# Kernel tuning notes

Measured on AMD Instinct MI355X. Metric: run time of the kernel, lower is better.

Reference implementation:

```python
import jax, jax.numpy as jnp
import numpy as np
from jax import lax

NUM_STEPS = 20
BATCH, DIM, HID = 4096, 512, 2048


def setup_inputs() -> dict:
    key = jax.random.key(0)
    k_z, k_w1, k_w2 = jax.random.split(key, 3)
    z0 = jax.random.normal(k_z, (BATCH, DIM), dtype=jnp.float32)
    # fan-in scaled weights so the ODE dynamics stay well-conditioned
    W1 = jax.random.normal(k_w1, (DIM + 1, HID), dtype=jnp.float32) * (1.0 / np.sqrt(DIM + 1))
    b1 = jnp.zeros((HID,), dtype=jnp.float32)
    W2 = jax.random.normal(k_w2, (HID, DIM), dtype=jnp.float32) * (0.1 / np.sqrt(HID))
    b2 = jnp.zeros((DIM,), dtype=jnp.float32)
    t0 = jnp.zeros((), dtype=jnp.float32)
    t1 = jnp.ones((), dtype=jnp.float32)
    return {"z0": z0, "W1": W1, "b1": b1, "W2": W2, "b2": b2, "t0": t0, "t1": t1}


def reference(z0, W1, b1, W2, b2, t0, t1):
    h = (t1 - t0) / NUM_STEPS

    def func(z, t):
        # time broadcast to [batch, 1], concatenated to the state (Neural-ODE MLP dynamics)
        tb = jnp.full((z.shape[0], 1), t, dtype=z.dtype)
        hidden = jnp.tanh(jnp.concatenate([z, tb], axis=-1) @ W1 + b1)
        return hidden @ W2 + b2

    def step(z, i):
        t = t0 + i * h
        k1 = func(z, t)
        k2 = func(z + 0.5 * h * k1, t + 0.5 * h)
        k3 = func(z + 0.5 * h * k2, t + 0.5 * h)
        k4 = func(z + h * k3, t + h)
        z_next = z + (h / 6.0) * (k1 + 2.0 * k2 + 2.0 * k3 + k4)
        return z_next, None

    z, _ = lax.scan(step, z0, jnp.arange(NUM_STEPS, dtype=z0.dtype))
    return z
```

## Files before the change

kernel.cpp:

```cpp
#include <hip/hip_runtime.h>
#include <hip/hip_bf16.h>

#define BATCH 4096
#define DIM   512
#define HID   2048
#define NSTEPS 20

typedef __attribute__((ext_vector_type(8))) short short8;
typedef __attribute__((ext_vector_type(4))) short short4v;
typedef __attribute__((ext_vector_type(4))) float floatx4;

#define GLL(dst, src) __builtin_amdgcn_global_load_lds( \
    (const __attribute__((address_space(1))) void*)(src), \
    (__attribute__((address_space(3))) void*)(dst), 16, 0, 0)

__device__ __forceinline__ short f2bf(float x) {
    union { float f; unsigned u; } v; v.f = x;
    unsigned r = v.u + 0x7fffu + ((v.u >> 16) & 1u);
    return (short)(r >> 16);
}

__device__ __forceinline__ float fast_tanh(float x) {
    float e = __builtin_amdgcn_exp2f(x * 2.8853900817779268f);
    float r = __builtin_amdgcn_rcpf(1.0f + e);
    return 1.0f - 2.0f * r;
}

__global__ void transpose_cvt(const float* __restrict__ src, short* __restrict__ dst,
                              int K, int N) {
    __shared__ float tile[32][33];
    int k0 = blockIdx.x * 32, n0 = blockIdx.y * 32;
    int tx = threadIdx.x, ty = threadIdx.y;
    #pragma unroll
    for (int r = ty; r < 32; r += 8)
        tile[r][tx] = src[(size_t)(k0 + r) * N + n0 + tx];
    __syncthreads();
    #pragma unroll
    for (int r = ty; r < 32; r += 8)
        dst[(size_t)(n0 + r) * K + k0 + tx] = f2bf(tile[tx][r]);
}

__global__ void extract_row(const float* __restrict__ W1, float* __restrict__ w1last) {
    int i = blockIdx.x * 256 + threadIdx.x;
    w1last[i] = W1[(size_t)DIM * HID + i];
}

__global__ void init_abuf(const float* __restrict__ z0, short* __restrict__ abuf) {
    size_t i = (size_t)(blockIdx.x * 256 + threadIdx.x) * 4;
    float4 zv = *(const float4*)(z0 + i);
    short4v o;
    o[0] = f2bf(zv.x); o[1] = f2bf(zv.y); o[2] = f2bf(zv.z); o[3] = f2bf(zv.w);
    *(short4v*)(abuf + i) = o;
}

__global__ __launch_bounds__(256, 2)
void gemm1_tanh(const short* __restrict__ A, const short* __restrict__ Bt,
                const float* __restrict__ b1, const float* __restrict__ w1last,
                const float* __restrict__ t0p, const float* __restrict__ t1p,
                float c_t, float step_i,
                short* __restrict__ hidden) {
    __shared__ short Alds[128 * 128];
    __shared__ short Blds[128 * 128];
    const int tid = threadIdx.x;
    const int lane = tid & 63;
    const int wave = tid >> 6;
    const int wm = wave >> 1, wn = wave & 1;
    const int bm0 = blockIdx.x * 128;
    const int bn0 = blockIdx.y * 128;

    const float t0 = t0p[0], t1 = t1p[0];
    const float h = (t1 - t0) / (float)NSTEPS;
    const float teval = t0 + (step_i + c_t) * h;

    floatx4 acc[4][4];
    #pragma unroll
    for (int i = 0; i < 4; i++)
        #pragma unroll
        for (int j = 0; j < 4; j++) acc[i][j] = (floatx4)0.f;

    const int fr = lane & 15;
    const int fkc = lane >> 4;
    const int rx = fr & 7;

    for (int kk = 0; kk < DIM; kk += 128) {
        #pragma unroll
        for (int p = 0; p < 8; p++) {
            int c = tid + p * 256;
            int row = c >> 4;
            int ci = c & 15;
            int g = ((ci & 7) ^ (row & 7)) | (ci & 8);
            GLL(&Alds[c * 8], A  + (size_t)(bm0 + row) * DIM + kk + g * 8);
            GLL(&Blds[c * 8], Bt + (size_t)(bn0 + row) * DIM + kk + g * 8);
        }
        __syncthreads();
        #pragma unroll
        for (int s = 0; s < 4; s++) {
            const int lc = s * 4 + fkc;
            const int slot = ((((lc & 7) ^ rx) | (lc & 8))) * 8;
            short8 af[4], bfr[4];
            #pragma unroll
            for (int mt = 0; mt < 4; mt++)
                af[mt] = *(const short8*)&Alds[(wm * 64 + mt * 16 + fr) * 128 + slot];
            #pragma unroll
            for (int nt = 0; nt < 4; nt++)
                bfr[nt] = *(const short8*)&Blds[(wn * 64 + nt * 16 + fr) * 128 + slot];
            #pragma unroll
            for (int mt = 0; mt < 4; mt++)
                #pragma unroll
                for (int nt = 0; nt < 4; nt++)
                    acc[mt][nt] = __builtin_amdgcn_mfma_f32_16x16x32_bf16(bfr[nt], af[mt], acc[mt][nt], 0, 0, 0);
        }
        __syncthreads();
    }
    #pragma unroll
    for (int mt = 0; mt < 4; mt++) {
        int m = bm0 + wm * 64 + mt * 16 + fr;
        short* hrow = hidden + (size_t)m * HID;
        #pragma unroll
        for (int nt = 0; nt < 4; nt++) {
            int n0 = bn0 + wn * 64 + nt * 16 + fkc * 4;
            float4 bb = *(const float4*)&b1[n0];
            float4 wl = *(const float4*)&w1last[n0];
            short4v o;
            o[0] = f2bf(fast_tanh(acc[mt][nt][0] + bb.x + teval * wl.x));
            o[1] = f2bf(fast_tanh(acc[mt][nt][1] + bb.y + teval * wl.y));
            o[2] = f2bf(fast_tanh(acc[mt][nt][2] + bb.z + teval * wl.z));
            o[3] = f2bf(fast_tanh(acc[mt][nt][3] + bb.w + teval * wl.w));
            *(short4v*)&hrow[n0] = o;
        }
    }
}

__global__ __launch_bounds__(512, 2)
void gemm2_fused(const short* __restrict__ hidden,
                 const short* __restrict__ Bt,
                 const float* __restrict__ b2,
                 float* __restrict__ z,
                 float* __restrict__ kacc, short* __restrict__ abuf,
                 const float* __restrict__ t0p, const float* __restrict__ t1p,
                 int mode, float wk, float alpha_c) {
    __shared__ short lds[8 * 8192];
    const int tid = threadIdx.x;
    const int lane = tid & 63;
    const int wave = tid >> 6;
    const int bm0 = blockIdx.x * 64;
    const int bn0 = blockIdx.y * 64;
    const int kbase = wave * 256;

    short* slabA = &lds[wave * 8192];
    short* slabB = slabA + 4096;

    const int fr = lane & 15;
    const int fkc = lane >> 4;
    const int rx = fr & 7;
    const int l3 = lane >> 3;
    const int gch = (lane & 7) ^ l3;

    floatx4 acc[4][4];
    #pragma unroll
    for (int i = 0; i < 4; i++)
        #pragma unroll
        for (int j = 0; j < 4; j++) acc[i][j] = (floatx4)0.f;

    #pragma unroll
    for (int it = 0; it < 4; ++it) {
        const int k0 = kbase + it * 64;
        __builtin_amdgcn_s_waitcnt(0xC07F);
        #pragma unroll
        for (int j = 0; j < 8; j++) {
            int row = j * 8 + l3;
            GLL(&slabA[j * 512 + lane * 8], hidden + (size_t)(bm0 + row) * HID + k0 + gch * 8);
            GLL(&slabB[j * 512 + lane * 8], Bt     + (size_t)(bn0 + row) * HID + k0 + gch * 8);
        }
        __builtin_amdgcn_sched_barrier(0);
        __builtin_amdgcn_s_waitcnt(0x0F70);
        __builtin_amdgcn_sched_barrier(0);
        #pragma unroll
        for (int s = 0; s < 2; s++) {
            const int slot = ((s * 4 + fkc) ^ rx) * 8;
            short8 af[4], bfr[4];
            #pragma unroll
            for (int mt = 0; mt < 4; mt++)
                af[mt] = *(const short8*)&slabA[(mt * 16 + fr) * 64 + slot];
            #pragma unroll
            for (int nt = 0; nt < 4; nt++)
                bfr[nt] = *(const short8*)&slabB[(nt * 16 + fr) * 64 + slot];
            #pragma unroll
            for (int mt = 0; mt < 4; mt++)
                #pragma unroll
                for (int nt = 0; nt < 4; nt++)
                    acc[mt][nt] = __builtin_amdgcn_mfma_f32_16x16x32_bf16(af[mt], bfr[nt], acc[mt][nt], 0, 0, 0);
        }
        __builtin_amdgcn_sched_barrier(0);
    }

    float* fslab = (float*)slabA;
    #pragma unroll
    for (int mt = 0; mt < 4; mt++)
        #pragma unroll
        for (int nt = 0; nt < 4; nt++)
            #pragma unroll
            for (int r = 0; r < 4; r++) {
                int row = mt * 16 + fkc * 4 + r;
                int col = nt * 16 + fr;
                fslab[row * 64 + col] = acc[mt][nt][r];
            }
    __syncthreads();

    const int rrow = tid >> 3;
    const int c8 = (tid & 7) * 8;
    float4 v0 = make_float4(0.f, 0.f, 0.f, 0.f);
    float4 v1 = make_float4(0.f, 0.f, 0.f, 0.f);
    #pragma unroll
    for (int w = 0; w < 8; w++) {
        const float* fs = (const float*)&lds[w * 8192];
        float4 p0 = *(const float4*)&fs[rrow * 64 + c8];
        float4 p1 = *(const float4*)&fs[rrow * 64 + c8 + 4];
        v0.x += p0.x; v0.y += p0.y; v0.z += p0.z; v0.w += p0.w;
        v1.x += p1.x; v1.y += p1.y; v1.z += p1.z; v1.w += p1.w;
    }

    const float h = (t1p[0] - t0p[0]) / (float)NSTEPS;
    const float ah = alpha_c * h;
    const float h6 = h / 6.0f;
    const size_t base = (size_t)(bm0 + rrow) * DIM + bn0 + c8;
    float4 bb0 = *(const float4*)&b2[bn0 + c8];
    float4 bb1 = *(const float4*)&b2[bn0 + c8 + 4];
    float kv[8] = { v0.x + bb0.x, v0.y + bb0.y, v0.z + bb0.z, v0.w + bb0.w,
                    v1.x + bb1.x, v1.y + bb1.y, v1.z + bb1.z, v1.w + bb1.w };
    float4 zv0 = *(const float4*)&z[base];
    float4 zv1 = *(const float4*)&z[base + 4];
    float zl[8] = { zv0.x, zv0.y, zv0.z, zv0.w, zv1.x, zv1.y, zv1.z, zv1.w };
    float zn[8];
    if (mode == 0) {
        *(float4*)&kacc[base]     = make_float4(kv[0], kv[1], kv[2], kv[3]);
        *(float4*)&kacc[base + 4] = make_float4(kv[4], kv[5], kv[6], kv[7]);
        #pragma unroll
        for (int i = 0; i < 8; i++) zn[i] = zl[i] + ah * kv[i];
    } else if (mode == 1) {
        float4 ka0 = *(const float4*)&kacc[base];
        float4 ka1 = *(const float4*)&kacc[base + 4];
        *(float4*)&kacc[base]     = make_float4(ka0.x + wk * kv[0], ka0.y + wk * kv[1],
                                                ka0.z + wk * kv[2], ka0.w + wk * kv[3]);
        *(float4*)&kacc[base + 4] = make_float4(ka1.x + wk * kv[4], ka1.y + wk * kv[5],
                                                ka1.z + wk * kv[6], ka1.w + wk * kv[7]);
        #pragma unroll
        for (int i = 0; i < 8; i++) zn[i] = zl[i] + ah * kv[i];
    } else {
        float4 ka0 = *(const float4*)&kacc[base];
        float4 ka1 = *(const float4*)&kacc[base + 4];
        float kaf[8] = { ka0.x, ka0.y, ka0.z, ka0.w, ka1.x, ka1.y, ka1.z, ka1.w };
        #pragma unroll
        for (int i = 0; i < 8; i++) zn[i] = zl[i] + h6 * (kaf[i] + kv[i]);
        *(float4*)&z[base]     = make_float4(zn[0], zn[1], zn[2], zn[3]);
        *(float4*)&z[base + 4] = make_float4(zn[4], zn[5], zn[6], zn[7]);
    }
    short4v o0, o1;
    o0[0] = f2bf(zn[0]); o0[1] = f2bf(zn[1]); o0[2] = f2bf(zn[2]); o0[3] = f2bf(zn[3]);
    o1[0] = f2bf(zn[4]); o1[1] = f2bf(zn[5]); o1[2] = f2bf(zn[6]); o1[3] = f2bf(zn[7]);
    *(short4v*)&abuf[base]     = o0;
    *(short4v*)&abuf[base + 4] = o1;
}

extern "C" void kernel_launch(void* const* d_in, const int* in_sizes, int n_in,
                              void* d_out, int out_size, void* d_ws, size_t ws_size,
                              hipStream_t stream) {
    const float* z0  = (const float*)d_in[0];
    const float* W1  = (const float*)d_in[1];
    const float* b1  = (const float*)d_in[2];
    const float* W2  = (const float*)d_in[3];
    const float* b2  = (const float*)d_in[4];
    const float* t0p = (const float*)d_in[5];
    const float* t1p = (const float*)d_in[6];
    float* z = (float*)d_out;

    char* ws = (char*)d_ws;
    short* W1t    = (short*)(ws);
    short* W2t    = (short*)(ws + (2u << 20));
    float* w1last = (float*)(ws + (4u << 20));
    short* abuf   = (short*)(ws + (4u << 20) + (1u << 16));
    short* hidden = (short*)(ws + (8u << 20) + (1u << 16));
    float* kacc   = (float*)(ws + (24u << 20) + (1u << 16));

    hipMemcpyAsync(z, z0, (size_t)BATCH * DIM * sizeof(float),
                   hipMemcpyDeviceToDevice, stream);
    transpose_cvt<<<dim3(DIM / 32, HID / 32), dim3(32, 8), 0, stream>>>(W1, W1t, DIM, HID);
    transpose_cvt<<<dim3(HID / 32, DIM / 32), dim3(32, 8), 0, stream>>>(W2, W2t, HID, DIM);
    extract_row<<<HID / 256, 256, 0, stream>>>(W1, w1last);
    init_abuf<<<BATCH * DIM / 4 / 256, 256, 0, stream>>>(z0, abuf);

    const dim3 g1(BATCH / 128, HID / 128), g2(BATCH / 64, DIM / 64);
    const dim3 b1d(256), b2d(512);
    for (int i = 0; i < NSTEPS; i++) {
        float fi = (float)i;
        gemm1_tanh<<<g1, b1d, 0, stream>>>(abuf, W1t, b1, w1last, t0p, t1p, 0.0f, fi, hidden);
        gemm2_fused<<<g2, b2d, 0, stream>>>(hidden, W2t, b2, z, kacc, abuf, t0p, t1p, 0, 1.0f, 0.5f);
        gemm1_tanh<<<g1, b1d, 0, stream>>>(abuf, W1t, b1, w1last, t0p, t1p, 0.5f, fi, hidden);
        gemm2_fused<<<g2, b2d, 0, stream>>>(hidden, W2t, b2, z, kacc, abuf, t0p, t1p, 1, 2.0f, 0.5f);
        gemm1_tanh<<<g1, b1d, 0, stream>>>(abuf, W1t, b1, w1last, t0p, t1p, 0.5f, fi, hidden);
        gemm2_fused<<<g2, b2d, 0, stream>>>(hidden, W2t, b2, z, kacc, abuf, t0p, t1p, 1, 2.0f, 1.0f);
        gemm1_tanh<<<g1, b1d, 0, stream>>>(abuf, W1t, b1, w1last, t0p, t1p, 1.0f, fi, hidden);
        gemm2_fused<<<g2, b2d, 0, stream>>>(hidden, W2t, b2, z, kacc, abuf, t0p, t1p, 2, 1.0f, 0.0f);
    }
}
```

Before: 2.958 ms.

## Halve gemm2 LDS footprint to fit more blocks per CU

The split-K gemm2 kernel now stages K-chunks of 32 instead of 64 per wave, which halves its LDS allocation. It also splits the cross-wave reduction epilogue into two column halves that reuse the smaller slabs, and raises the launch-bounds occupancy hint from 2 to 4 blocks. The aim is to fit more resident blocks per CU and hide global-load latency. In exchange there are twice as many load/wait iterations, an extra barrier, and the XOR swizzle is dropped, which may cause LDS bank conflicts on the fragment reads.

After: 3.394 ms. 1.15x slower.

```diff
diff --git a/kernel.cpp b/kernel.cpp
--- a/kernel.cpp
+++ b/kernel.cpp
@@ -131,7 +131,7 @@
     }
 }
 
-__global__ __launch_bounds__(512, 2)
+__global__ __launch_bounds__(512, 4)
 void gemm2_fused(const short* __restrict__ hidden,
                  const short* __restrict__ Bt,
                  const float* __restrict__ b2,
@@ -139,7 +139,7 @@
                  float* __restrict__ kacc, short* __restrict__ abuf,
                  const float* __restrict__ t0p, const float* __restrict__ t1p,
                  int mode, float wk, float alpha_c) {
-    __shared__ short lds[8 * 8192];
+    __shared__ short lds[8 * 4096];
     const int tid = threadIdx.x;
     const int lane = tid & 63;
     const int wave = tid >> 6;
@@ -147,14 +147,11 @@
     const int bn0 = blockIdx.y * 64;
     const int kbase = wave * 256;
 
-    short* slabA = &lds[wave * 8192];
-    short* slabB = slabA + 4096;
+    short* slabA = &lds[wave * 4096];
+    short* slabB = slabA + 2048;
 
     const int fr = lane & 15;
     const int fkc = lane >> 4;
-    const int rx = fr & 7;
-    const int l3 = lane >> 3;
-    const int gch = (lane & 7) ^ l3;
 
     floatx4 acc[4][4];
     #pragma unroll
@@ -163,28 +160,28 @@
         for (int j = 0; j < 4; j++) acc[i][j] = (floatx4)0.f;
 
     #pragma unroll
-    for (int it = 0; it < 4; ++it) {
-        const int k0 = kbase + it * 64;
+    for (int it = 0; it < 8; ++it) {
+        const int k0 = kbase + it * 32;
         __builtin_amdgcn_s_waitcnt(0xC07F);
         #pragma unroll
-        for (int j = 0; j < 8; j++) {
-            int row = j * 8 + l3;
-            GLL(&slabA[j * 512 + lane * 8], hidden + (size_t)(bm0 + row) * HID + k0 + gch * 8);
-            GLL(&slabB[j * 512 + lane * 8], Bt     + (size_t)(bn0 + row) * HID + k0 + gch * 8);
+        for (int p = 0; p < 4; p++) {
+            int c = lane + p * 64;
+            int row = c >> 2;
+            int kc = c & 3;
+            GLL(&slabA[c * 8], hidden + (size_t)(bm0 + row) * HID + k0 + kc * 8);
+            GLL(&slabB[c * 8], Bt     + (size_t)(bn0 + row) * HID + k0 + kc * 8);
         }
         __builtin_amdgcn_sched_barrier(0);
         __builtin_amdgcn_s_waitcnt(0x0F70);
         __builtin_amdgcn_sched_barrier(0);
-        #pragma unroll
-        for (int s = 0; s < 2; s++) {
-            const int slot = ((s * 4 + fkc) ^ rx) * 8;
+        {
             short8 af[4], bfr[4];
             #pragma unroll
             for (int mt = 0; mt < 4; mt++)
-                af[mt] = *(const short8*)&slabA[(mt * 16 + fr) * 64 + slot];
+                af[mt] = *(const short8*)&slabA[(mt * 16 + fr) * 32 + fkc * 8];
             #pragma unroll
             for (int nt = 0; nt < 4; nt++)
-                bfr[nt] = *(const short8*)&slabB[(nt * 16 + fr) * 64 + slot];
+                bfr[nt] = *(const short8*)&slabB[(nt * 16 + fr) * 32 + fkc * 8];
             #pragma unroll
             for (int mt = 0; mt < 4; mt++)
                 #pragma unroll
@@ -194,72 +191,69 @@
         __builtin_amdgcn_sched_barrier(0);
     }
 
-    float* fslab = (float*)slabA;
-    #pragma unroll
-    for (int mt = 0; mt < 4; mt++)
-        #pragma unroll
-        for (int nt = 0; nt < 4; nt++)
-            #pragma unroll
-            for (int r = 0; r < 4; r++) {
-                int row = mt * 16 + fkc * 4 + r;
-                int col = nt * 16 + fr;
-                fslab[row * 64 + col] = acc[mt][nt][r];
-            }
-    __syncthreads();
-
-    const int rrow = tid >> 3;
-    const int c8 = (tid & 7) * 8;
-    float4 v0 = make_float4(0.f, 0.f, 0.f, 0.f);
-    float4 v1 = make_float4(0.f, 0.f, 0.f, 0.f);
-    #pragma unroll
-    for (int w = 0; w < 8; w++) {
-        const float* fs = (const float*)&lds[w * 8192];
-        float4 p0 = *(const float4*)&fs[rrow * 64 + c8];
-        float4 p1 = *(const float4*)&fs[rrow * 64 + c8 + 4];
-        v0.x += p0.x; v0.y += p0.y; v0.z += p0.z; v0.w += p0.w;
-        v1.x += p1.x; v1.y += p1.y; v1.z += p1.z; v1.w += p1.w;
-    }
+    __builtin_amdgcn_s_waitcnt(0xC07F);
 
     const float h = (t1p[0] - t0p[0]) / (float)NSTEPS;
     const float ah = alpha_c * h;
     const float h6 = h / 6.0f;
-    const size_t base = (size_t)(bm0 + rrow) * DIM + bn0 + c8;
-    float4 bb0 = *(const float4*)&b2[bn0 + c8];
-    float4 bb1 = *(const float4*)&b2[bn0 + c8 + 4];
-    float kv[8] = { v0.x + bb0.x, v0.y + bb0.y, v0.z + bb0.z, v0.w + bb0.w,
-                    v1.x + bb1.x, v1.y + bb1.y, v1.z + bb1.z, v1.w + bb1.w };
-    float4 zv0 = *(const float4*)&z[base];
-    float4 zv1 = *(const float4*)&z[base + 4];
-    float zl[8] = { zv0.x, zv0.y, zv0.z, zv0.w, zv1.x, zv1.y, zv1.z, zv1.w };
-    float zn[8];
-    if (mode == 0) {
-        *(float4*)&kacc[base]     = make_float4(kv[0], kv[1], kv[2], kv[3]);
-        *(float4*)&kacc[base + 4] = make_float4(kv[4], kv[5], kv[6], kv[7]);
-        #pragma unroll
-        for (int i = 0; i < 8; i++) zn[i] = zl[i] + ah * kv[i];
-    } else if (mode == 1) {
-        float4 ka0 = *(const float4*)&kacc[base];
-        float4 ka1 = *(const float4*)&kacc[base + 4];
-        *(float4*)&kacc[base]     = make_float4(ka0.x + wk * kv[0], ka0.y + wk * kv[1],
-                                                ka0.z + wk * kv[2], ka0.w + wk * kv[3]);
-        *(float4*)&kacc[base + 4] = make_float4(ka1.x + wk * kv[4], ka1.y + wk * kv[5],
-                                                ka1.z + wk * kv[6], ka1.w + wk * kv[7]);
-        #pragma unroll
-        for (int i = 0; i < 8; i++) zn[i] = zl[i] + ah * kv[i];
-    } else {
-        float4 ka0 = *(const float4*)&kacc[base];
-        float4 ka1 = *(const float4*)&kacc[base + 4];
-        float kaf[8] = { ka0.x, ka0.y, ka0.z, ka0.w, ka1.x, ka1.y, ka1.z, ka1.w };
-        #pragma unroll
-        for (int i = 0; i < 8; i++) zn[i] = zl[i] + h6 * (kaf[i] + kv[i]);
-        *(float4*)&z[base]     = make_float4(zn[0], zn[1], zn[2], zn[3]);
-        *(float4*)&z[base + 4] = make_float4(zn[4], zn[5], zn[6], zn[7]);
-    }
-    short4v o0, o1;
-    o0[0] = f2bf(zn[0]); o0[1] = f2bf(zn[1]); o0[2] = f2bf(zn[2]); o0[3] = f2bf(zn[3]);
-    o1[0] = f2bf(zn[4]); o1[1] = f2bf(zn[5]); o1[2] = f2bf(zn[6]); o1[3] = f2bf(zn[7]);
-    *(short4v*)&abuf[base]     = o0;
-    *(short4v*)&abuf[base + 4] = o1;
+    const int rrow = tid >> 3;
+    const int c4 = (tid & 7) * 4;
+
+    #pragma unroll
+    for (int c2 = 0; c2 < 2; ++c2) {
+        if (c2 == 1) __syncthreads();
+        float* fslab = (float*)slabA;
+        #pragma unroll
+        for (int mt = 0; mt < 4; mt++)
+            #pragma unroll
+            for (int ntl = 0; ntl < 2; ntl++) {
+                const int nt = c2 * 2 + ntl;
+                #pragma unroll
+                for (int r = 0; r < 4; r++) {
+                    int row = mt * 16 + fkc * 4 + r;
+                    int colw = ntl * 16 + fr;
+                    fslab[row * 32 + colw] = acc[mt][nt][r];
+                }
+            }
+        __syncthreads();
+
+        float4 v = make_float4(0.f, 0.f, 0.f, 0.f);
+        #pragma unroll
+        for (int w = 0; w < 8; w++) {
+            const float* fs = (const float*)&lds[w * 4096];
+            float4 p = *(const float4*)&fs[rrow * 32 + c4];
+            v.x += p.x; v.y += p.y; v.z += p.z; v.w += p.w;
+        }
+
+        const int ncol = bn0 + c2 * 32 + c4;
+        const size_t base = (size_t)(bm0 + rrow) * DIM + ncol;
+        float4 bb = *(const float4*)&b2[ncol];
+        float kv[4] = { v.x + bb.x, v.y + bb.y, v.z + bb.z, v.w + bb.w };
+        float4 zq = *(const float4*)&z[base];
+        float zl[4] = { zq.x, zq.y, zq.z, zq.w };
+        float zn[4];
+        if (mode == 0) {
+            *(float4*)&kacc[base] = make_float4(kv[0], kv[1], kv[2], kv[3]);
+            #pragma unroll
+            for (int i = 0; i < 4; i++) zn[i] = zl[i] + ah * kv[i];
+        } else if (mode == 1) {
+            float4 ka = *(const float4*)&kacc[base];
+            *(float4*)&kacc[base] = make_float4(ka.x + wk * kv[0], ka.y + wk * kv[1],
+                                                ka.z + wk * kv[2], ka.w + wk * kv[3]);
+            #pragma unroll
+            for (int i = 0; i < 4; i++) zn[i] = zl[i] + ah * kv[i];
+        } else {
+            float4 ka = *(const float4*)&kacc[base];
+            zn[0] = zl[0] + h6 * (ka.x + kv[0]);
+            zn[1] = zl[1] + h6 * (ka.y + kv[1]);
+            zn[2] = zl[2] + h6 * (ka.z + kv[2]);
+            zn[3] = zl[3] + h6 * (ka.w + kv[3]);
+            *(float4*)&z[base] = make_float4(zn[0], zn[1], zn[2], zn[3]);
+        }
+        short4v o;
+        o[0] = f2bf(zn[0]); o[1] = f2bf(zn[1]); o[2] = f2bf(zn[2]); o[3] = f2bf(zn[3]);
+        *(short4v*)&abuf[base] = o;
+    }
 }
 
 extern "C" void kernel_launch(void* const* d_in, const int* in_sizes, int n_in,
@@ -282,8 +276,8 @@
     short* hidden = (short*)(ws + (8u << 20) + (1u << 16));
     float* kacc   = (float*)(ws + (24u << 20) + (1u << 16));
 
-    hipMemcpyAsync(z, z0, (size_t)BATCH * DIM * sizeof(float),
-                   hipMemcpyDeviceToDevice, stream);
+    (void)hipMemcpyAsync(z, z0, (size_t)BATCH * DIM * sizeof(float),
+                         hipMemcpyDeviceToDevice, stream);
     transpose_cvt<<<dim3(DIM / 32, HID / 32), dim3(32, 8), 0, stream>>>(W1, W1t, DIM, HID);
     transpose_cvt<<<dim3(HID / 32, DIM / 32), dim3(32, 8), 0, stream>>>(W2, W2t, HID, DIM);
     extract_row<<<HID / 256, 256, 0, stream>>>(W1, w1last);
```
